# Optimization experiments

Measured on AMD Instinct MI355X. Metric: run time of the kernel, lower is better.

The kernel has to match this reference:

```python
import jax, jax.numpy as jnp
import numpy as np

N_EMBED = 256
HEAD_SIZE = 64


def setup_inputs() -> dict:
    key = jax.random.key(0)
    ks = jax.random.split(key, 8)
    B, N, C, H = 4, 16384, N_EMBED, HEAD_SIZE
    inp = {
        "x0": jax.random.normal(ks[0], (B, N, C), dtype=jnp.float32),
        "x1": jax.random.normal(ks[1], (B, N, C), dtype=jnp.float32),
    }
    # torch nn.Linear weights: [out, in], y = x @ W.T (no bias, qkv_bias=False)
    scale = 1.0 / np.sqrt(C)
    names = ["Wk0", "Wk1", "Wq0", "Wq1", "Wv0", "Wv1"]
    for i, n in enumerate(names):
        inp[n] = jax.random.uniform(ks[2 + i], (H, C), dtype=jnp.float32,
                                    minval=-scale, maxval=scale)
    return inp


def reference(x0, x1, Wk0, Wk1, Wq0, Wq1, Wv0, Wv1):
    # projections: [B, N, C] @ [C, H] -> [B, N, H]
    k0 = jnp.einsum("bnc,hc->bnh", x0, Wk0)
    k1 = jnp.einsum("bnc,hc->bnh", x1, Wk1)
    q0 = jnp.einsum("bnc,hc->bnh", x0, Wq0)
    q1 = jnp.einsum("bnc,hc->bnh", x1, Wq1)
    v0 = jnp.einsum("bnc,hc->bnh", x0, Wv0)
    v1 = jnp.einsum("bnc,hc->bnh", x1, Wv1)
    # softmax over tokens (axis=-2) for keys, over head dim (-1) for queries
    k0 = jax.nn.softmax(k0, axis=-2)
    k1 = jax.nn.softmax(k1, axis=-2)
    q0 = jax.nn.softmax(q0, axis=-1)
    q1 = jax.nn.softmax(q1, axis=-1)
    # context matrices: [B, H, H]
    w0 = jnp.einsum("bnh,bnd->bhd", k0, v0)
    w1 = jnp.einsum("bnh,bnd->bhd", k1, v1)
    # cross attention outputs: [B, N, H]
    attn_x0 = jnp.einsum("bnh,bhd->bnd", q0, w1)
    attn_x1 = jnp.einsum("bnh,bhd->bnd", q1, w0)
    return (attn_x0, attn_x1)
```

## Files before the change

### kernel.cpp

```cpp
#include <hip/hip_runtime.h>


#define B_ 4
#define N_ 16384
#define C_ 256

typedef float f32x4 __attribute__((ext_vector_type(4)));
typedef __bf16 bf16x8 __attribute__((ext_vector_type(8)));
typedef __bf16 bf16x4v __attribute__((ext_vector_type(4)));
typedef unsigned short us8 __attribute__((ext_vector_type(8)));

__device__ __forceinline__ unsigned short f2bf(float f) {
  union { float f; unsigned u; } v; v.f = f;
  return (unsigned short)((v.u + 0x7FFFu + ((v.u >> 16) & 1u)) >> 16);
}
__device__ __forceinline__ float bf2f(unsigned short h) {
  union { unsigned u; float f; } v; v.u = ((unsigned)h) << 16;
  return v.f;
}

__device__ __forceinline__ void sync_lds() {
  asm volatile("s_waitcnt lgkmcnt(0)" ::: "memory");
  __builtin_amdgcn_sched_barrier(0);
  __builtin_amdgcn_s_barrier();
  __builtin_amdgcn_sched_barrier(0);
}

__device__ __forceinline__ void load_lds16(const void* g, void* l) {
  __builtin_amdgcn_global_load_lds(
      (const __attribute__((address_space(1))) unsigned int*)g,
      (__attribute__((address_space(3))) unsigned int*)l, 16, 0, 0);
}

#define WPACK_OFF 0u
#define Q_OFF     262144u
#define PNW_OFF   17039360u
#define PZ_OFF    33816576u
#define WFIN_OFF  34340864u

__global__ __launch_bounds__(256) void kW_pack(
    const float* __restrict__ Wk0, const float* __restrict__ Wk1,
    const float* __restrict__ Wq0, const float* __restrict__ Wq1,
    const float* __restrict__ Wv0, const float* __restrict__ Wv1,
    unsigned short* __restrict__ wpack) {
  int t = blockIdx.x * 256 + threadIdx.x;
  int i = t & 7;
  int lane = (t >> 3) & 63;
  int q = t >> 9;
  int ks = q & 7;
  int sj = q >> 3;
  int s = sj / 12;
  int j = sj - s * 12;
  int gc = 16 * j + (lane & 15);
  int c = 32 * ks + ((lane >> 4) << 3) + i;
  int m = gc >> 6, row = gc & 63;
  const float* W;
  if (s == 0) W = (m == 0) ? Wk0 : (m == 1) ? Wq0 : Wv0;
  else        W = (m == 0) ? Wk1 : (m == 1) ? Wq1 : Wv1;
  wpack[t] = f2bf(W[row * 256 + c]);
}

__global__ __launch_bounds__(256, 2) void kP_proj(
    const float* __restrict__ x0, const float* __restrict__ x1,
    const unsigned short* __restrict__ wpack,
    unsigned short* __restrict__ qbuf, unsigned short* __restrict__ pnw,
    float* __restrict__ pz) {
  int slot = blockIdx.x;
  int bs = blockIdx.y;
  int b = bs >> 1, s = bs & 1;
  const float* x = (s ? x1 : x0) + (size_t)b * N_ * C_;
  int t = threadIdx.x;
  int w = t >> 6;
  int l = t & 63;
  int l15 = l & 15, lg = l >> 4;

  __shared__ __align__(16) char lds[79872];
  char* xfA = lds;
  char* xfB = lds + 32768;
  char* pTb = lds + 65536;
  char* vTb = lds + 70656;
  char* qsb = lds + 75776;

  const char* wbase = (const char*)wpack + (size_t)s * 12 * 8 * 64 * 16;

  bf16x8 bfr[3][8];
#pragma unroll
  for (int jj = 0; jj < 3; ++jj)
#pragma unroll
    for (int ks = 0; ks < 8; ++ks)
      bfr[jj][ks] = *(const bf16x8*)(wbase + (((size_t)((w + 4*jj)*8 + ks))*64 + l)*16);
#pragma unroll
  for (int jj = 0; jj < 3; ++jj)
#pragma unroll
    for (int ks = 0; ks < 8; ++ks)
      asm volatile("" : "+v"(bfr[jj][ks]));

  f32x4 nwacc[4];
#pragma unroll
  for (int df = 0; df < 4; ++df) { f32x4 z = {0.f,0.f,0.f,0.f}; nwacc[df] = z; }
  float zacc = 0.f;

  auto STAGE = [&](int tile, char* buf) {
    int nn0 = slot * 256 + tile * 32;
    const char* xgb = (const char*)(x + (size_t)nn0 * C_);
#pragma unroll
    for (int i = 0; i < 8; ++i) {
      int f = t + 256 * i;
      int row = f >> 6;
      int srcoff = (f * 16) ^ ((row & 7) << 4);
      load_lds16(xgb + srcoff, buf + f * 16);
    }
  };

  STAGE(0, xfA);
  asm volatile("s_waitcnt vmcnt(0)" ::: "memory");
  sync_lds();

#pragma unroll 1
  for (int it = 0; it < 8; ++it) {
    int n0 = slot * 256 + it * 32;
    char* xb = (it & 1) ? xfB : xfA;
    char* xn = (it & 1) ? xfA : xfB;

    if (it < 7) STAGE(it + 1, xn);

    f32x4 acc[2][3];
#pragma unroll
    for (int rf = 0; rf < 2; ++rf)
#pragma unroll
      for (int jj = 0; jj < 3; ++jj) { f32x4 z = {0.f,0.f,0.f,0.f}; acc[rf][jj] = z; }

    __builtin_amdgcn_s_setprio(1);
#pragma unroll
    for (int ks = 0; ks < 8; ++ks) {
      bf16x8 a[2];
#pragma unroll
      for (int rf = 0; rf < 2; ++rf) {
        int row = rf * 16 + l15;
        int off = row * 1024 + ks * 128 + lg * 32;
        int so = off ^ ((row & 7) << 4);
        f32x4 v0 = *(const f32x4*)(xb + so);
        f32x4 v1 = *(const f32x4*)(xb + (so ^ 16));
        bf16x8 av;
        av[0] = (__bf16)v0[0]; av[1] = (__bf16)v0[1];
        av[2] = (__bf16)v0[2]; av[3] = (__bf16)v0[3];
        av[4] = (__bf16)v1[0]; av[5] = (__bf16)v1[1];
        av[6] = (__bf16)v1[2]; av[7] = (__bf16)v1[3];
        a[rf] = av;
      }
#pragma unroll
      for (int jj = 0; jj < 3; ++jj)
#pragma unroll
        for (int rf = 0; rf < 2; ++rf)
          acc[rf][jj] = __builtin_amdgcn_mfma_f32_16x16x32_bf16(
              a[rf], bfr[jj][ks], acc[rf][jj], 0, 0, 0);
    }
    __builtin_amdgcn_s_setprio(0);


    {
      int hcol = w * 16 + l15;
#pragma unroll
      for (int rf = 0; rf < 2; ++rf) {
        float e0 = __expf(acc[rf][0][0]), e1 = __expf(acc[rf][0][1]);
        float e2 = __expf(acc[rf][0][2]), e3 = __expf(acc[rf][0][3]);
        zacc += e0 + e1 + e2 + e3;
        bf16x4v pk;
        pk[0] = (__bf16)e0; pk[1] = (__bf16)e1;
        pk[2] = (__bf16)e2; pk[3] = (__bf16)e3;
        *(bf16x4v*)(pTb + hcol * 80 + (rf * 16 + lg * 4) * 2) = pk;
      }
    }
    {
      int dcol = w * 16 + l15;
#pragma unroll
      for (int rf = 0; rf < 2; ++rf) {
        bf16x4v pk;
        pk[0] = (__bf16)acc[rf][2][0]; pk[1] = (__bf16)acc[rf][2][1];
        pk[2] = (__bf16)acc[rf][2][2]; pk[3] = (__bf16)acc[rf][2][3];
        *(bf16x4v*)(vTb + dcol * 80 + (rf * 16 + lg * 4) * 2) = pk;
      }
    }
    {
#pragma unroll
      for (int rf = 0; rf < 2; ++rf)
#pragma unroll
        for (int r = 0; r < 4; ++r) {
          int n = rf * 16 + lg * 4 + r;
          int off = (n * 128 + (w * 16 + l15) * 2) ^ ((n & 7) << 4);
          *(__bf16*)(qsb + off) = (__bf16)acc[rf][1][r];
        }
    }
    sync_lds();

    {
      unsigned short* qg = qbuf + ((size_t)bs * N_ + n0) * 64;
      int n = t >> 3, c = t & 7;
      int off = (n * 128 + c * 16) ^ ((n & 7) << 4);
      us8 v = *(const us8*)(qsb + off);
      *(us8*)(qg + (size_t)t * 8) = v;
    }

    __builtin_amdgcn_s_setprio(1);
    {
      bf16x8 a2 = *(const bf16x8*)(pTb + (w * 16 + l15) * 80 + lg * 16);
#pragma unroll
      for (int df = 0; df < 4; ++df) {
        bf16x8 b2 = *(const bf16x8*)(vTb + (df * 16 + l15) * 80 + lg * 16);
        nwacc[df] = __builtin_amdgcn_mfma_f32_16x16x32_bf16(a2, b2, nwacc[df], 0, 0, 0);
      }
    }
    __builtin_amdgcn_s_setprio(0);

    asm volatile("s_waitcnt vmcnt(1)" ::: "memory");
    sync_lds();
  }

  {
    float zl = zacc;
    zl += __shfl_xor(zl, 16);
    zl += __shfl_xor(zl, 32);
    if (lg == 0)
      pz[((size_t)bs * 64 + slot) * 64 + w * 16 + l15] = zl;
  }

  {
    size_t base = ((size_t)bs * 64 + slot) * 4096;
#pragma unroll
    for (int df = 0; df < 4; ++df)
#pragma unroll
      for (int r = 0; r < 4; ++r) {
        int h = w * 16 + lg * 4 + r;
        int d = df * 16 + l15;
        pnw[base + h * 64 + d] = f2bf(nwacc[df][r]);
      }
  }
}

__global__ __launch_bounds__(256) void kB_reduce(
    const unsigned short* __restrict__ pnw, const float* __restrict__ pz,
    float* __restrict__ wfin) {
  int g = blockIdx.x;
  int bs = blockIdx.y;
  int t = threadIdx.x;
  int wv = t >> 6, l = t & 63;
  __shared__ float zinv[4];
  int h = g * 4 + wv;
  float z = pz[((size_t)bs * 64 + l) * 64 + h];
#pragma unroll
  for (int m = 32; m; m >>= 1) z += __shfl_xor(z, m);
  if (l == 0) zinv[wv] = 1.f / z;
  __syncthreads();
  int idx = g * 256 + t;
  float ssum = 0.f;
#pragma unroll 8
  for (int p = 0; p < 64; ++p)
    ssum += bf2f(pnw[((size_t)bs * 64 + p) * 4096 + idx]);
  wfin[(size_t)bs * 4096 + idx] = ssum * zinv[wv];
}

__global__ __launch_bounds__(256) void kC_out(
    const unsigned short* __restrict__ qbuf, const float* __restrict__ wfin,
    float* __restrict__ out) {
  int bs = blockIdx.y, b = bs >> 1, s = bs & 1;
  int t = threadIdx.x;
  int w = t >> 6, l = t & 63;
  int l15 = l & 15, lg = l >> 4;
  int tok0 = blockIdx.x * 64;

  __shared__ __align__(16) char cb[16384];
  char* plb = cb;
  char* wlb = cb + 8192;
  float* ob = (float*)cb;

  const float* wsrc = wfin + (size_t)(b * 2 + (1 - s)) * 4096;
#pragma unroll
  for (int rr = 0; rr < 4; ++rr) {
    int fi = t + 256 * rr;
    int h = fi >> 4, d4 = (fi & 15) * 4;
    f32x4 v = *(const f32x4*)(wsrc + h * 64 + d4);
#pragma unroll
    for (int e = 0; e < 4; ++e) {
      int d = d4 + e;
      int off = (d * 128 + h * 2) ^ ((d & 7) << 4);
      *(unsigned short*)(wlb + off) = f2bf(v[e]);
    }
  }

  {
    int tl = t >> 2, p4 = t & 3;
    const unsigned short* qr =
        qbuf + ((size_t)bs * N_ + tok0 + tl) * 64 + p4 * 16;
    us8 u0 = *(const us8*)(qr);
    us8 u1 = *(const us8*)(qr + 8);
    float e[16]; float sum = 0.f;
#pragma unroll
    for (int i = 0; i < 8; ++i) { e[i] = __expf(bf2f(u0[i])); sum += e[i]; }
#pragma unroll
    for (int i = 0; i < 8; ++i) { e[8+i] = __expf(bf2f(u1[i])); sum += e[8+i]; }
    sum += __shfl_xor(sum, 1);
    sum += __shfl_xor(sum, 2);
    float inv = 1.f / sum;
    us8 p0, p1;
#pragma unroll
    for (int i = 0; i < 8; ++i) { p0[i] = f2bf(e[i] * inv); p1[i] = f2bf(e[8+i] * inv); }
    int off = (tl * 128 + p4 * 32) ^ ((tl & 7) << 4);
    *(us8*)(plb + off) = p0;
    *(us8*)(plb + (off ^ 16)) = p1;
  }
  __syncthreads();

  f32x4 acc[4];
#pragma unroll
  for (int rf = 0; rf < 4; ++rf) { f32x4 z = {0.f,0.f,0.f,0.f}; acc[rf] = z; }
#pragma unroll
  for (int k2 = 0; k2 < 2; ++k2) {
    int dd = w * 16 + l15;
    int boff = (dd * 128 + (k2 * 32 + lg * 8) * 2) ^ ((dd & 7) << 4);
    bf16x8 bfrag = *(const bf16x8*)(wlb + boff);
#pragma unroll
    for (int rf = 0; rf < 4; ++rf) {
      int row = rf * 16 + l15;
      int aoff = (row * 128 + (k2 * 32 + lg * 8) * 2) ^ ((row & 7) << 4);
      bf16x8 afrag = *(const bf16x8*)(plb + aoff);
      acc[rf] = __builtin_amdgcn_mfma_f32_16x16x32_bf16(afrag, bfrag, acc[rf], 0, 0, 0);
    }
  }
  __syncthreads();

#pragma unroll
  for (int rf = 0; rf < 4; ++rf)
#pragma unroll
    for (int r = 0; r < 4; ++r) {
      int tok = rf * 16 + lg * 4 + r;
      int d = w * 16 + l15;
      ob[tok * 64 + d] = acc[rf][r];
    }
  __syncthreads();

  float* outp = out + (size_t)s * ((size_t)B_ * N_ * 64) +
                ((size_t)b * N_ + tok0) * 64;
#pragma unroll
  for (int r2 = 0; r2 < 4; ++r2) {
    int fi = t + 256 * r2;
    ((f32x4*)outp)[fi] = ((const f32x4*)ob)[fi];
  }
}

extern "C" void kernel_launch(void* const* d_in, const int* in_sizes, int n_in,
                              void* d_out, int out_size, void* d_ws, size_t ws_size,
                              hipStream_t stream) {
  const float* x0  = (const float*)d_in[0];
  const float* x1  = (const float*)d_in[1];
  const float* Wk0 = (const float*)d_in[2];
  const float* Wk1 = (const float*)d_in[3];
  const float* Wq0 = (const float*)d_in[4];
  const float* Wq1 = (const float*)d_in[5];
  const float* Wv0 = (const float*)d_in[6];
  const float* Wv1 = (const float*)d_in[7];
  float* out = (float*)d_out;
  char* wsb = (char*)d_ws;
  unsigned short* wpack = (unsigned short*)(wsb + WPACK_OFF);
  unsigned short* qbuf  = (unsigned short*)(wsb + Q_OFF);
  unsigned short* pnw   = (unsigned short*)(wsb + PNW_OFF);
  float* pz   = (float*)(wsb + PZ_OFF);
  float* wfin = (float*)(wsb + WFIN_OFF);

  kW_pack<<<dim3(384), dim3(256), 0, stream>>>(Wk0, Wk1, Wq0, Wq1, Wv0, Wv1, wpack);
  kP_proj<<<dim3(64, 8), dim3(256), 0, stream>>>(x0, x1, wpack, qbuf, pnw, pz);
  kB_reduce<<<dim3(16, 8), dim3(256), 0, stream>>>(pnw, pz, wfin);
  kC_out<<<dim3(256, 8), dim3(256), 0, stream>>>(qbuf, wfin, out);
}
```

Baseline: 52.69 us.

## Double-buffer P/V/Q LDS tiles and defer context MFMA by one iteration

Splits the P, V and Q staging areas in LDS into two ping-pong buffers. The Q global store and the context MFMA for tile it-1 now run inside iteration it, which removes the second barrier per loop iteration and lets that work overlap the exp/convert stage; a short epilogue handles the last tile. In exchange, LDS per block grows from about 78 KB to about 92 KB. That likely no longer lets two blocks share a CU as the launch bounds ask, which would halve occupancy for a 512-block grid.

```diff
diff --git a/kernel.cpp b/kernel.cpp
--- a/kernel.cpp
+++ b/kernel.cpp
@@ -74,12 +74,15 @@
   int l = t & 63;
   int l15 = l & 15, lg = l >> 4;
 
-  __shared__ __align__(16) char lds[79872];
+  __shared__ __align__(16) char lds[94208];
   char* xfA = lds;
   char* xfB = lds + 32768;
-  char* pTb = lds + 65536;
-  char* vTb = lds + 70656;
-  char* qsb = lds + 75776;
+  char* pT0 = lds + 65536;
+  char* vT0 = lds + 70656;
+  char* qs0 = lds + 75776;
+  char* pT1 = lds + 79872;
+  char* vT1 = lds + 84992;
+  char* qs1 = lds + 90112;
 
   const char* wbase = (const char*)wpack + (size_t)s * 12 * 8 * 64 * 16;
 
@@ -118,9 +121,14 @@
 
 #pragma unroll 1
   for (int it = 0; it < 8; ++it) {
-    int n0 = slot * 256 + it * 32;
     char* xb = (it & 1) ? xfB : xfA;
     char* xn = (it & 1) ? xfA : xfB;
+    char* ovPw = (it & 1) ? pT1 : pT0;
+    char* ovVw = (it & 1) ? vT1 : vT0;
+    char* ovQw = (it & 1) ? qs1 : qs0;
+    char* ovPr = (it & 1) ? pT0 : pT1;
+    char* ovVr = (it & 1) ? vT0 : vT1;
+    char* ovQr = (it & 1) ? qs0 : qs1;
 
     if (it < 7) STAGE(it + 1, xn);
 
@@ -157,6 +165,23 @@
     }
     __builtin_amdgcn_s_setprio(0);
 
+    if (it >= 1) {
+      int n0p = slot * 256 + (it - 1) * 32;
+      unsigned short* qg = qbuf + ((size_t)bs * N_ + n0p) * 64;
+      int n = t >> 3, c = t & 7;
+      int off = (n * 128 + c * 16) ^ ((n & 7) << 4);
+      us8 v = *(const us8*)(ovQr + off);
+      *(us8*)(qg + (size_t)t * 8) = v;
+
+      __builtin_amdgcn_s_setprio(1);
+      bf16x8 a2 = *(const bf16x8*)(ovPr + (w * 16 + l15) * 80 + lg * 16);
+#pragma unroll
+      for (int df = 0; df < 4; ++df) {
+        bf16x8 b2 = *(const bf16x8*)(ovVr + (df * 16 + l15) * 80 + lg * 16);
+        nwacc[df] = __builtin_amdgcn_mfma_f32_16x16x32_bf16(a2, b2, nwacc[df], 0, 0, 0);
+      }
+      __builtin_amdgcn_s_setprio(0);
+    }
 
     {
       int hcol = w * 16 + l15;
@@ -168,7 +193,7 @@
         bf16x4v pk;
         pk[0] = (__bf16)e0; pk[1] = (__bf16)e1;
         pk[2] = (__bf16)e2; pk[3] = (__bf16)e3;
-        *(bf16x4v*)(pTb + hcol * 80 + (rf * 16 + lg * 4) * 2) = pk;
+        *(bf16x4v*)(ovPw + hcol * 80 + (rf * 16 + lg * 4) * 2) = pk;
       }
     }
     {
@@ -178,7 +203,7 @@
         bf16x4v pk;
         pk[0] = (__bf16)acc[rf][2][0]; pk[1] = (__bf16)acc[rf][2][1];
         pk[2] = (__bf16)acc[rf][2][2]; pk[3] = (__bf16)acc[rf][2][3];
-        *(bf16x4v*)(vTb + dcol * 80 + (rf * 16 + lg * 4) * 2) = pk;
+        *(bf16x4v*)(ovVw + dcol * 80 + (rf * 16 + lg * 4) * 2) = pk;
       }
     }
     {
@@ -188,32 +213,29 @@
         for (int r = 0; r < 4; ++r) {
           int n = rf * 16 + lg * 4 + r;
           int off = (n * 128 + (w * 16 + l15) * 2) ^ ((n & 7) << 4);
-          *(__bf16*)(qsb + off) = (__bf16)acc[rf][1][r];
+          *(__bf16*)(ovQw + off) = (__bf16)acc[rf][1][r];
         }
     }
+
+    if (it == 0) asm volatile("s_waitcnt vmcnt(0)" ::: "memory");
+    else         asm volatile("s_waitcnt vmcnt(1)" ::: "memory");
     sync_lds();
-
-    {
-      unsigned short* qg = qbuf + ((size_t)bs * N_ + n0) * 64;
-      int n = t >> 3, c = t & 7;
-      int off = (n * 128 + c * 16) ^ ((n & 7) << 4);
-      us8 v = *(const us8*)(qsb + off);
-      *(us8*)(qg + (size_t)t * 8) = v;
-    }
-
-    __builtin_amdgcn_s_setprio(1);
-    {
-      bf16x8 a2 = *(const bf16x8*)(pTb + (w * 16 + l15) * 80 + lg * 16);
-#pragma unroll
-      for (int df = 0; df < 4; ++df) {
-        bf16x8 b2 = *(const bf16x8*)(vTb + (df * 16 + l15) * 80 + lg * 16);
-        nwacc[df] = __builtin_amdgcn_mfma_f32_16x16x32_bf16(a2, b2, nwacc[df], 0, 0, 0);
-      }
-    }
-    __builtin_amdgcn_s_setprio(0);
-
-    asm volatile("s_waitcnt vmcnt(1)" ::: "memory");
-    sync_lds();
+  }
+
+  {
+    int n0p = slot * 256 + 7 * 32;
+    unsigned short* qg = qbuf + ((size_t)bs * N_ + n0p) * 64;
+    int n = t >> 3, c = t & 7;
+    int off = (n * 128 + c * 16) ^ ((n & 7) << 4);
+    us8 v = *(const us8*)(qs1 + off);
+    *(us8*)(qg + (size_t)t * 8) = v;
+
+    bf16x8 a2 = *(const bf16x8*)(pT1 + (w * 16 + l15) * 80 + lg * 16);
+#pragma unroll
+    for (int df = 0; df < 4; ++df) {
+      bf16x8 b2 = *(const bf16x8*)(vT1 + (df * 16 + l15) * 80 + lg * 16);
+      nwacc[df] = __builtin_amdgcn_mfma_f32_16x16x32_bf16(a2, b2, nwacc[df], 0, 0, 0);
+    }
   }
 
   {
```

Result: slower. 58.14 us (+10.3%).
